# Performance work log

Measured on AMD Instinct MI355X. Metric: run time of the kernel, lower is better.

Reference implementation:

```python
import jax, jax.numpy as jnp
import numpy as np

B, S, D, H = 8, 1024, 1024, 16
DK = D // H
EPS = 1e-5

def _layernorm(x, w, b):
    mu = jnp.mean(x, axis=-1, keepdims=True)
    var = jnp.mean((x - mu) ** 2, axis=-1, keepdims=True)
    return (x - mu) * jax.lax.rsqrt(var + EPS) * w + b

def setup_inputs() -> dict:
    key = jax.random.key(0)
    ks = jax.random.split(key, 12)
    x = jax.random.normal(ks[0], (B, S, D), dtype=jnp.float32)
    batch_lengths = jax.random.randint(ks[1], (B,), S // 2, S + 1, dtype=jnp.int32)
    sc = 1.0 / np.sqrt(D)
    Wq = jax.random.normal(ks[2], (H, D, DK), dtype=jnp.float32) * sc
    Wk = jax.random.normal(ks[3], (H, D, DK), dtype=jnp.float32) * sc
    Wv = jax.random.normal(ks[4], (H, D, DK), dtype=jnp.float32) * sc
    fc1_w = jax.random.normal(ks[5], (D, D), dtype=jnp.float32) * sc
    fc1_b = jnp.zeros((D,), dtype=jnp.float32)
    fc2_w = jax.random.normal(ks[6], (D, D), dtype=jnp.float32) * sc
    fc2_b = jnp.zeros((D,), dtype=jnp.float32)
    ln1_w = jnp.ones((D,), dtype=jnp.float32)
    ln1_b = jnp.zeros((D,), dtype=jnp.float32)
    ln2_w = jnp.ones((D,), dtype=jnp.float32)
    ln2_b = jnp.zeros((D,), dtype=jnp.float32)
    return {"x": x, "Wq": Wq, "Wk": Wk, "Wv": Wv, "fc1_w": fc1_w, "fc1_b": fc1_b,
            "fc2_w": fc2_w, "fc2_b": fc2_b, "ln1_w": ln1_w, "ln1_b": ln1_b,
            "ln2_w": ln2_w, "ln2_b": ln2_b, "batch_lengths": batch_lengths, "max_len": S}

def reference(x, Wq, Wk, Wv, fc1_w, fc1_b, fc2_w, fc2_b, ln1_w, ln1_b, ln2_w, ln2_b, batch_lengths, max_len):
    b, s, d = x.shape
    h, _, dk = Wq.shape
    # padding masks: valid positions are t < length
    row = (jnp.arange(s)[None, :] < batch_lengths[:, None]).astype(x.dtype)  # [B,S]
    m = row[:, :, None]                 # [B,S,1], outputMask per-row
    mh = m[:, None]                     # [B,1,S,1]
    # all heads batched: Q,K,V -> [B,H,S,dk], masked like Wq(ctx)*mask etc.
    Q = jnp.einsum('bsd,hde->bhse', x, Wq) * mh
    K = jnp.einsum('bsd,hde->bhse', x, Wk) * mh
    V = jnp.einsum('bsd,hde->bhse', x, Wv) * mh
    energy = jnp.einsum('bhqe,bhke->bhqk', Q, K)
    # attnMask: key columns beyond length -> -inf
    key_valid = row[:, None, None, :] > 0
    energy = jnp.where(key_valid, energy, -jnp.inf)
    score = jax.nn.softmax(energy / jnp.sqrt(jnp.asarray(dk, x.dtype)), axis=-1)
    z = jnp.einsum('bhqk,bhke->bhqe', score, V)           # [B,H,S,dk]
    z = z.transpose(0, 2, 1, 3).reshape(b, s, d) * m      # concat heads, mask
    x1 = _layernorm(x + z, ln1_w, ln1_b)
    ff = jax.nn.relu(x1 @ fc1_w + fc1_b) * m
    ff = (ff @ fc2_w + fc2_b) * m
    return _layernorm(x1 + ff, ln2_w, ln2_b)
```

## Files before the change

### kernel.cpp

```cpp
#include <hip/hip_runtime.h>
#include <math.h>

#define B_ 8
#define S_ 1024
#define D_ 1024
#define H_ 16
#define DK_ 64
#define EPS_ 1e-5f

typedef __bf16 bf16_t;
typedef __bf16 bf16x8 __attribute__((ext_vector_type(8)));
typedef __bf16 bf16x4v __attribute__((ext_vector_type(4)));
typedef float  f32x4  __attribute__((ext_vector_type(4)));

__device__ __forceinline__ void gld16(const void* g, void* l) {
    __builtin_amdgcn_global_load_lds(
        (const __attribute__((address_space(1))) void*)g,
        (__attribute__((address_space(3))) void*)l, 16, 0, 0);
}

__global__ __launch_bounds__(256)
void prep(const float* __restrict__ x,
          const float* __restrict__ Wq, const float* __restrict__ Wk,
          const float* __restrict__ Wv, const float* __restrict__ W1,
          const float* __restrict__ W2, bf16_t* __restrict__ xb,
          bf16_t* __restrict__ WtQKV, bf16_t* __restrict__ Wt1,
          bf16_t* __restrict__ Wt2)
{
    __shared__ float tile[64][65];
    const int tid = threadIdx.x;
    const int z = blockIdx.z;

    if (z >= 5) {
        const int blk = (z - 5) * 256 + blockIdx.y * 16 + blockIdx.x;
        const int i = (blk * 256 + tid) * 4;
        const float4 v = *(const float4*)(x + i);
        bf16x4v o = { (bf16_t)v.x, (bf16_t)v.y, (bf16_t)v.z, (bf16_t)v.w };
        *(bf16x4v*)(xb + i) = o;
        return;
    }

    const int n0 = blockIdx.x * 64, k0 = blockIdx.y * 64;
    const int col = tid & 63, r0 = tid >> 6;
    const float* src = (z == 0) ? Wq : (z == 1) ? Wk : (z == 2) ? Wv
                     : (z == 3) ? W1 : W2;
    #pragma unroll
    for (int i = 0; i < 16; i++) {
        const int row = r0 + i * 4;
        float v;
        if (z < 3)
            v = src[((size_t)(n0 >> 6) << 16) + (size_t)(k0 + row) * 64 + col];
        else
            v = src[(size_t)(k0 + row) * D_ + n0 + col];
        tile[row][col] = v;
    }
    __syncthreads();
    bf16_t* dst = (z < 3) ? (WtQKV + (size_t)z * D_ * D_)
                : (z == 3) ? Wt1 : Wt2;
    #pragma unroll
    for (int i = 0; i < 16; i++) {
        const int nr = r0 + i * 4;
        dst[(size_t)(n0 + nr) * D_ + k0 + col] = (bf16_t)tile[col][nr];
    }
}

template<int EPI, typename OUT>
__global__ __launch_bounds__(256)
void gemm_mfma(const bf16_t* __restrict__ A, const bf16_t* __restrict__ Bw,
               const float* __restrict__ bias, const int* __restrict__ lens,
               OUT* __restrict__ C, int M, int N, int K)
{
    __shared__ bf16_t As[128 * 32];
    __shared__ bf16_t Bs[128 * 32];
    const int tid  = threadIdx.x;
    const int lane = tid & 63;
    const int w    = tid >> 6;
    const int quad = lane >> 4, l16 = lane & 15;
    const int wm = w & 1, wn = w >> 1;
    const int bn = blockIdx.x * 128, bm = blockIdx.y * 128;

    f32x4 acc[4][4];
    #pragma unroll
    for (int i = 0; i < 4; i++)
        #pragma unroll
        for (int j = 0; j < 4; j++)
            #pragma unroll
            for (int r = 0; r < 4; r++) acc[i][j][r] = 0.f;

    const int fsw = (quad ^ (l16 ^ (l16 >> 2))) & 3;

    for (int k0 = 0; k0 < K; k0 += 32) {
        #pragma unroll
        for (int j = 0; j < 2; j++) {
            const int chunk = j * 256 + tid;
            const int m = chunk >> 2, cs = chunk & 3;
            const int cg = cs ^ ((m ^ (m >> 2)) & 3);
            gld16(A + (size_t)(bm + m) * K + k0 + cg * 8,
                  (char*)As + (size_t)(j * 256 + w * 64) * 16);
            gld16(Bw + (size_t)(bn + m) * K + k0 + cg * 8,
                  (char*)Bs + (size_t)(j * 256 + w * 64) * 16);
        }
        __syncthreads();

        bf16x8 a[4], b[4];
        #pragma unroll
        for (int i = 0; i < 4; i++)
            a[i] = *(const bf16x8*)&As[(wm * 64 + i * 16 + l16) * 32 + fsw * 8];
        #pragma unroll
        for (int j = 0; j < 4; j++)
            b[j] = *(const bf16x8*)&Bs[(wn * 64 + j * 16 + l16) * 32 + fsw * 8];
        #pragma unroll
        for (int i = 0; i < 4; i++)
            #pragma unroll
            for (int j = 0; j < 4; j++)
                acc[i][j] = __builtin_amdgcn_mfma_f32_16x16x32_bf16(a[i], b[j], acc[i][j], 0, 0, 0);
        __syncthreads();
    }

    #pragma unroll
    for (int i = 0; i < 4; i++) {
        #pragma unroll
        for (int r = 0; r < 4; r++) {
            const int m = bm + wm * 64 + i * 16 + quad * 4 + r;
            float keep = 1.f;
            if (EPI != 0) {
                const int s = m & (S_ - 1);
                const int bb = m >> 10;
                keep = (s < lens[bb]) ? 1.f : 0.f;
            }
            #pragma unroll
            for (int j = 0; j < 4; j++) {
                const int n = bn + wn * 64 + j * 16 + l16;
                float v = acc[i][j][r];
                if (EPI != 0) {
                    v += bias[n];
                    if (EPI == 1) v = fmaxf(v, 0.f);
                    v *= keep;
                }
                C[(size_t)m * N + n] = (OUT)v;
            }
        }
    }
}

__global__ __launch_bounds__(256, 3)
void attn_mfma(const bf16_t* __restrict__ QKV, const int* __restrict__ lens,
               bf16_t* __restrict__ Z)
{
    __shared__ __align__(16) bf16_t Ks[2][64][64];
    __shared__ __align__(16) bf16_t Vt[2][64][72];
    __shared__ __align__(16) bf16_t Ps[64][72];

    const int tid  = threadIdx.x;
    const int lane = tid & 63;
    const int w    = tid >> 6;
    const int quad = lane >> 4;
    const int l16  = lane & 15;
    const int id   = blockIdx.x;
    const int b    = id & 7;
    const int h    = (id >> 3) & 15;
    const int qt   = id >> 7;
    const int len  = lens[b];
    const int qbase = qt * 64;
    const bf16_t* Qp = QKV + (size_t)b * S_ * 3072 + (size_t)h * 64;
    const bf16_t* Kp = Qp + 1024;
    const bf16_t* Vp = Qp + 2048;
    const size_t zbase = (size_t)b * S_ * D_ + (size_t)h * 64;

    if (qbase >= len) {
        const int r = tid >> 2, c0 = (tid & 3) * 16;
        bf16_t* zp = Z + zbase + (size_t)(qbase + r) * D_ + c0;
        uint4 zz = {0u, 0u, 0u, 0u};
        *(uint4*)zp = zz;
        *(uint4*)(zp + 8) = zz;
        return;
    }

    const int qrow = qbase + w * 16 + l16;
    const bf16x8 bq0 = *(const bf16x8*)(Qp + (size_t)qrow * 3072 + quad * 8);
    const bf16x8 bq1 = *(const bf16x8*)(Qp + (size_t)qrow * 3072 + 32 + quad * 8);

    const int kr0  = tid >> 3;
    const int kpos = tid & 7;
    const int kc0  = (kpos ^ (kr0 & 7)) << 3;
    const int kc1  = (kpos ^ ((kr0 + 32) & 7)) << 3;

    const int vr  = tid >> 2;
    const int vc0 = (tid & 3) * 16;
    const int vp  = vr ^ ((tid & 3) << 4);

    f32x4 o[4];
    #pragma unroll
    for (int dm = 0; dm < 4; dm++)
        #pragma unroll
        for (int r = 0; r < 4; r++) o[dm][r] = 0.f;
    float l_q = 0.f;

    const int ntiles = (len + 63) >> 6;

    gld16(Kp + (size_t)kr0 * 3072 + kc0,
          (char*)&Ks[0][0][0] + (size_t)(w * 64) * 16);
    gld16(Kp + (size_t)(kr0 + 32) * 3072 + kc1,
          (char*)&Ks[0][0][0] + (size_t)(256 + w * 64) * 16);
    bf16x8 vcur0 = *(const bf16x8*)(Vp + (size_t)vr * 3072 + vc0);
    bf16x8 vcur1 = *(const bf16x8*)(Vp + (size_t)vr * 3072 + vc0 + 8);
    __syncthreads();

    for (int t = 0; t < ntiles; t++) {
        const int k0 = t * 64;
        const int cb = t & 1, nb = (t + 1) & 1;
        const int kn0 = (t + 1 < ntiles ? t + 1 : t) * 64;

        gld16(Kp + (size_t)(kn0 + kr0) * 3072 + kc0,
              (char*)&Ks[nb][0][0] + (size_t)(w * 64) * 16);
        gld16(Kp + (size_t)(kn0 + kr0 + 32) * 3072 + kc1,
              (char*)&Ks[nb][0][0] + (size_t)(256 + w * 64) * 16);
        const bf16_t* vsrc = Vp + (size_t)(kn0 + vr) * 3072 + vc0;
        const bf16x8 vn0 = *(const bf16x8*)vsrc;
        const bf16x8 vn1 = *(const bf16x8*)(vsrc + 8);
        __builtin_amdgcn_sched_barrier(0);

        #pragma unroll
        for (int kt = 0; kt < 4; kt++) {
            const int r = kt * 16 + l16;
            const bf16x8 ak0 = *(const bf16x8*)&Ks[cb][r][(quad ^ (l16 & 7)) << 3];
            const bf16x8 ak1 = *(const bf16x8*)&Ks[cb][r][((4 + quad) ^ (l16 & 7)) << 3];
            f32x4 z4 = {0.f, 0.f, 0.f, 0.f};
            z4 = __builtin_amdgcn_mfma_f32_16x16x32_bf16(ak0, bq0, z4, 0, 0, 0);
            const f32x4 sfv = __builtin_amdgcn_mfma_f32_16x16x32_bf16(ak1, bq1, z4, 0, 0, 0);
            bf16x4v pk;
            #pragma unroll
            for (int r2 = 0; r2 < 4; r2++) {
                const int key = k0 + kt * 16 + quad * 4 + r2;
                float p = __expf(sfv[r2] * 0.125f);
                p = (key < len) ? p : 0.f;
                l_q += p;
                pk[r2] = (bf16_t)p;
            }
            *(bf16x4v*)&Ps[w * 16 + l16][kt * 16 + quad * 4] = pk;
        }

        #pragma unroll
        for (int i = 0; i < 8; i++) Vt[cb][vc0 + i][vp] = vcur0[i];
        #pragma unroll
        for (int i = 0; i < 8; i++) Vt[cb][vc0 + 8 + i][vp] = vcur1[i];
        vcur0 = vn0;
        vcur1 = vn1;
        __syncthreads();

        const bf16x8 bp0 = *(const bf16x8*)&Ps[w * 16 + l16][quad * 8];
        const bf16x8 bp1 = *(const bf16x8*)&Ps[w * 16 + l16][32 + quad * 8];
        #pragma unroll
        for (int dm = 0; dm < 4; dm++) {
            const bf16x8 av0 = *(const bf16x8*)&Vt[cb][dm * 16 + l16][(quad * 8) ^ (dm * 16)];
            const bf16x8 av1 = *(const bf16x8*)&Vt[cb][dm * 16 + l16][(32 + quad * 8) ^ (dm * 16)];
            o[dm] = __builtin_amdgcn_mfma_f32_16x16x32_bf16(av0, bp0, o[dm], 0, 0, 0);
            o[dm] = __builtin_amdgcn_mfma_f32_16x16x32_bf16(av1, bp1, o[dm], 0, 0, 0);
        }
    }

    l_q += __shfl_xor(l_q, 16);
    l_q += __shfl_xor(l_q, 32);
    const int qg = qbase + w * 16 + l16;
    const float inv = (qg < len) ? 1.f / l_q : 0.f;
    bf16_t* zrow = Z + zbase + (size_t)qg * D_;
    #pragma unroll
    for (int dm = 0; dm < 4; dm++) {
        bf16x4v st;
        #pragma unroll
        for (int r = 0; r < 4; r++) st[r] = (bf16_t)(o[dm][r] * inv);
        *(bf16x4v*)(zrow + dm * 16 + quad * 4) = st;
    }
}

__device__ __forceinline__ void ln_core(float vx, float vy, float vz, float vw,
                                        int tid, float& mean, float& rstd)
{
    __shared__ float red[8];
    float s = vx + vy + vz + vw;
    #pragma unroll
    for (int off = 32; off; off >>= 1) s += __shfl_xor(s, off, 64);
    const int wv = tid >> 6, lane = tid & 63;
    if (lane == 0) red[wv] = s;
    __syncthreads();
    mean = (red[0] + red[1] + red[2] + red[3]) * (1.f / D_);
    const float dx = vx - mean, dy = vy - mean, dz = vz - mean, dw = vw - mean;
    float s2 = dx * dx + dy * dy + dz * dz + dw * dw;
    #pragma unroll
    for (int off = 32; off; off >>= 1) s2 += __shfl_xor(s2, off, 64);
    if (lane == 0) red[4 + wv] = s2;
    __syncthreads();
    rstd = rsqrtf((red[4] + red[5] + red[6] + red[7]) * (1.f / D_) + EPS_);
}

__global__ __launch_bounds__(256)
void add_ln1(const float* __restrict__ X, const bf16_t* __restrict__ Y,
             const float* __restrict__ g, const float* __restrict__ beta,
             bf16_t* __restrict__ out)
{
    const int row = blockIdx.x, tid = threadIdx.x;
    const float4 xv = ((const float4*)(X + (size_t)row * D_))[tid];
    const bf16x4v yv = *(const bf16x4v*)(Y + (size_t)row * D_ + tid * 4);
    const float vx = xv.x + (float)yv[0], vy = xv.y + (float)yv[1];
    const float vz = xv.z + (float)yv[2], vw = xv.w + (float)yv[3];
    float mean, rstd;
    ln_core(vx, vy, vz, vw, tid, mean, rstd);
    const float4 gv = ((const float4*)g)[tid];
    const float4 bv = ((const float4*)beta)[tid];
    bf16x4v o;
    o[0] = (bf16_t)((vx - mean) * rstd * gv.x + bv.x);
    o[1] = (bf16_t)((vy - mean) * rstd * gv.y + bv.y);
    o[2] = (bf16_t)((vz - mean) * rstd * gv.z + bv.z);
    o[3] = (bf16_t)((vw - mean) * rstd * gv.w + bv.w);
    *(bf16x4v*)(out + (size_t)row * D_ + tid * 4) = o;
}

__global__ __launch_bounds__(256)
void add_ln2(const bf16_t* __restrict__ X, const float* __restrict__ Y,
             const float* __restrict__ g, const float* __restrict__ beta,
             float* __restrict__ out)
{
    const int row = blockIdx.x, tid = threadIdx.x;
    const bf16x4v xv = *(const bf16x4v*)(X + (size_t)row * D_ + tid * 4);
    const float4 yv = ((const float4*)(Y + (size_t)row * D_))[tid];
    const float vx = (float)xv[0] + yv.x, vy = (float)xv[1] + yv.y;
    const float vz = (float)xv[2] + yv.z, vw = (float)xv[3] + yv.w;
    float mean, rstd;
    ln_core(vx, vy, vz, vw, tid, mean, rstd);
    const float4 gv = ((const float4*)g)[tid];
    const float4 bv = ((const float4*)beta)[tid];
    float4 o;
    o.x = (vx - mean) * rstd * gv.x + bv.x;
    o.y = (vy - mean) * rstd * gv.y + bv.y;
    o.z = (vz - mean) * rstd * gv.z + bv.z;
    o.w = (vw - mean) * rstd * gv.w + bv.w;
    ((float4*)(out + (size_t)row * D_))[tid] = o;
}

extern "C" void kernel_launch(void* const* d_in, const int* in_sizes, int n_in,
                              void* d_out, int out_size, void* d_ws, size_t ws_size,
                              hipStream_t stream)
{
    const float* x    = (const float*)d_in[0];
    const float* Wq   = (const float*)d_in[1];
    const float* Wk   = (const float*)d_in[2];
    const float* Wv   = (const float*)d_in[3];
    const float* fc1w = (const float*)d_in[4];
    const float* fc1b = (const float*)d_in[5];
    const float* fc2w = (const float*)d_in[6];
    const float* fc2b = (const float*)d_in[7];
    const float* ln1w = (const float*)d_in[8];
    const float* ln1b = (const float*)d_in[9];
    const float* ln2w = (const float*)d_in[10];
    const float* ln2b = (const float*)d_in[11];
    const int*   lens = (const int*)d_in[12];
    float* out = (float*)d_out;

    char* ws = (char*)d_ws;
    const size_t MB = 1024 * 1024;
    bf16_t* QKVb  = (bf16_t*)(ws);
    bf16_t* Zb    = (bf16_t*)(ws + 48 * MB);
    bf16_t* X1b   = (bf16_t*)(ws + 80 * MB);
    bf16_t* xb    = (bf16_t*)(ws + 96 * MB);
    bf16_t* H1b   = (bf16_t*)(ws + 96 * MB);
    float*  FF    = (float*)(ws + 48 * MB);
    bf16_t* WtQKV = (bf16_t*)(ws + 112 * MB);
    bf16_t* Wt1   = (bf16_t*)(ws + 118 * MB);
    bf16_t* Wt2   = (bf16_t*)(ws + 120 * MB);

    const int M = B_ * S_;

    prep<<<dim3(16, 16, 37), 256, 0, stream>>>(x, Wq, Wk, Wv, fc1w, fc2w,
                                               xb, WtQKV, Wt1, Wt2);

    gemm_mfma<0, bf16_t><<<dim3(3072 / 128, M / 128), 256, 0, stream>>>(
        xb, WtQKV, nullptr, nullptr, QKVb, M, 3072, D_);

    attn_mfma<<<dim3(2048), 256, 0, stream>>>(QKVb, lens, Zb);

    add_ln1<<<M, 256, 0, stream>>>(x, Zb, ln1w, ln1b, X1b);

    gemm_mfma<1, bf16_t><<<dim3(D_ / 128, M / 128), 256, 0, stream>>>(
        X1b, Wt1, fc1b, lens, H1b, M, D_, D_);
    gemm_mfma<2, float><<<dim3(D_ / 128, M / 128), 256, 0, stream>>>(
        H1b, Wt2, fc2b, lens, FF, M, D_, D_);

    add_ln2<<<M, 256, 0, stream>>>(X1b, FF, ln2w, ln2b, out);
}
```

Before: 336.9 us.

## Replace GEMM with 256x256 double-buffered 8-wave pipelined MFMA kernel

Replaces the 128x128 single-buffered GEMM with a 256x256-tile, 512-thread kernel using BK=64. LDS is double-buffered with async global-to-LDS loads interleaved across four quarter-tile MFMA phases, with barrier and priority tricks. It aims to raise MFMA utilisation and hide load latency. In exchange it uses large LDS (limiting occupancy) and launches far fewer blocks, which underfills the CUs for the D×D FFN GEMMs.

```diff
diff --git a/kernel.cpp b/kernel.cpp
--- a/kernel.cpp
+++ b/kernel.cpp
@@ -65,63 +65,139 @@
 }
 
 template<int EPI, typename OUT>
-__global__ __launch_bounds__(256)
-void gemm_mfma(const bf16_t* __restrict__ A, const bf16_t* __restrict__ Bw,
-               const float* __restrict__ bias, const int* __restrict__ lens,
-               OUT* __restrict__ C, int M, int N, int K)
-{
-    __shared__ bf16_t As[128 * 32];
-    __shared__ bf16_t Bs[128 * 32];
+__global__ __launch_bounds__(512, 2)
+void gemm8(const bf16_t* __restrict__ A, const bf16_t* __restrict__ Bw,
+           const float* __restrict__ bias, const int* __restrict__ lens,
+           OUT* __restrict__ C, int M, int N, int K)
+{
+    __shared__ __align__(16) bf16_t As[2][256 * 64];
+    __shared__ __align__(16) bf16_t Bs[2][256 * 64];
+
     const int tid  = threadIdx.x;
     const int lane = tid & 63;
     const int w    = tid >> 6;
     const int quad = lane >> 4, l16 = lane & 15;
     const int wm = w & 1, wn = w >> 1;
-    const int bn = blockIdx.x * 128, bm = blockIdx.y * 128;
-
-    f32x4 acc[4][4];
-    #pragma unroll
-    for (int i = 0; i < 4; i++)
+    const int bn = blockIdx.x * 256, bm = blockIdx.y * 256;
+    const int sw8 = l16 & 7;
+
+    const int ci0 = tid, ci1 = tid + 512;
+    const int aB0 = ci0 >> 9, aR0 = (ci0 >> 3) & 63;
+    const int aC0 = (((ci0 & 7) ^ (aR0 & 7)) << 3);
+    const int aB1 = ci1 >> 9, aR1 = (ci1 >> 3) & 63;
+    const int aC1 = (((ci1 & 7) ^ (aR1 & 7)) << 3);
+    const int bB0 = ci0 >> 8, bR0 = (ci0 >> 3) & 31;
+    const int bC0 = (((ci0 & 7) ^ (bR0 & 7)) << 3);
+    const int bB1 = ci1 >> 8, bR1 = (ci1 >> 3) & 31;
+    const int bC1 = (((ci1 & 7) ^ (bR1 & 7)) << 3);
+    const int u0 = w * 64, u1 = 512 + w * 64;
+    const int adD0 = (u0 >> 9) * 16384 + (u0 & 511) * 16;
+    const int adD1 = (u1 >> 9) * 16384 + (u1 & 511) * 16;
+    const int bdD0 = (u0 >> 8) * 8192 + (u0 & 255) * 16;
+    const int bdD1 = (u1 >> 8) * 8192 + (u1 & 255) * 16;
+
+    f32x4 acc[8][4];
+    #pragma unroll
+    for (int i = 0; i < 8; i++)
         #pragma unroll
         for (int j = 0; j < 4; j++)
             #pragma unroll
             for (int r = 0; r < 4; r++) acc[i][j][r] = 0.f;
 
-    const int fsw = (quad ^ (l16 ^ (l16 >> 2))) & 3;
-
-    for (int k0 = 0; k0 < K; k0 += 32) {
-        #pragma unroll
-        for (int j = 0; j < 2; j++) {
-            const int chunk = j * 256 + tid;
-            const int m = chunk >> 2, cs = chunk & 3;
-            const int cg = cs ^ ((m ^ (m >> 2)) & 3);
-            gld16(A + (size_t)(bm + m) * K + k0 + cg * 8,
-                  (char*)As + (size_t)(j * 256 + w * 64) * 16);
-            gld16(Bw + (size_t)(bn + m) * K + k0 + cg * 8,
-                  (char*)Bs + (size_t)(j * 256 + w * 64) * 16);
-        }
-        __syncthreads();
-
-        bf16x8 a[4], b[4];
-        #pragma unroll
-        for (int i = 0; i < 4; i++)
-            a[i] = *(const bf16x8*)&As[(wm * 64 + i * 16 + l16) * 32 + fsw * 8];
-        #pragma unroll
-        for (int j = 0; j < 4; j++)
-            b[j] = *(const bf16x8*)&Bs[(wn * 64 + j * 16 + l16) * 32 + fsw * 8];
-        #pragma unroll
-        for (int i = 0; i < 4; i++)
-            #pragma unroll
-            for (int j = 0; j < 4; j++)
-                acc[i][j] = __builtin_amdgcn_mfma_f32_16x16x32_bf16(a[i], b[j], acc[i][j], 0, 0, 0);
-        __syncthreads();
-    }
-
-    #pragma unroll
-    for (int i = 0; i < 4; i++) {
+#define STAGE_A(h, nb_, kt_) { \
+    char* d_ = (char*)As[nb_] + (h) * 8192; \
+    gld16(A + (size_t)(bm + aB0 * 128 + (h) * 64 + aR0) * K + (kt_) * 64 + aC0, d_ + adD0); \
+    gld16(A + (size_t)(bm + aB1 * 128 + (h) * 64 + aR1) * K + (kt_) * 64 + aC1, d_ + adD1); }
+#define STAGE_B(h, nb_, kt_) { \
+    char* d_ = (char*)Bs[nb_] + (h) * 4096; \
+    gld16(Bw + (size_t)(bn + bB0 * 64 + (h) * 32 + bR0) * K + (kt_) * 64 + bC0, d_ + bdD0); \
+    gld16(Bw + (size_t)(bn + bB1 * 64 + (h) * 32 + bR1) * K + (kt_) * 64 + bC1, d_ + bdD1); }
+#define RD_A(dst, base, qm_, i_, kh_) \
+    dst = *(const bf16x8*)&base[(wm * 128 + (qm_) * 64 + (i_) * 16 + l16) * 64 + ((((kh_) * 4 + quad) ^ sw8) << 3)];
+#define RD_B(dst, base, qn_, j_, kh_) \
+    dst = *(const bf16x8*)&base[(wn * 64 + (qn_) * 32 + (j_) * 16 + l16) * 64 + ((((kh_) * 4 + quad) ^ sw8) << 3)];
+#define MM(QI, QJ, AF, BF) \
+    _Pragma("unroll") \
+    for (int kh_ = 0; kh_ < 2; kh_++) \
+        _Pragma("unroll") \
+        for (int i_ = 0; i_ < 4; i_++) \
+            _Pragma("unroll") \
+            for (int j_ = 0; j_ < 2; j_++) \
+                acc[(QI) * 4 + i_][(QJ) * 2 + j_] = __builtin_amdgcn_mfma_f32_16x16x32_bf16( \
+                    AF[i_][kh_], BF[j_][kh_], acc[(QI) * 4 + i_][(QJ) * 2 + j_], 0, 0, 0);
+#define MIDBAR() { __builtin_amdgcn_s_barrier(); \
+    asm volatile("s_waitcnt lgkmcnt(0)" ::: "memory"); }
+
+    const int NKT = K >> 6;
+
+    STAGE_A(0, 0, 0);
+    STAGE_B(0, 0, 0);
+    STAGE_B(1, 0, 0);
+    STAGE_A(1, 0, 0);
+    asm volatile("s_waitcnt vmcnt(4)" ::: "memory");
+    __builtin_amdgcn_s_barrier();
+
+    for (int t = 0; t < NKT; ++t) {
+        const int cb = t & 1, nb = cb ^ 1;
+        const int ktn = (t + 1 < NKT) ? t + 1 : t;
+        const bf16_t* Ac = As[cb];
+        const bf16_t* Bc = Bs[cb];
+
+        bf16x8 fa[4][2], fb[2][2];
+        #pragma unroll
+        for (int i = 0; i < 4; i++) { RD_A(fa[i][0], Ac, 0, i, 0); RD_A(fa[i][1], Ac, 0, i, 1); }
+        #pragma unroll
+        for (int j = 0; j < 2; j++) { RD_B(fb[j][0], Bc, 0, j, 0); RD_B(fb[j][1], Bc, 0, j, 1); }
+        STAGE_A(0, nb, ktn);
+        MIDBAR();
+        __builtin_amdgcn_s_setprio(1);
+        MM(0, 0, fa, fb);
+        __builtin_amdgcn_s_setprio(0);
+        asm volatile("s_waitcnt vmcnt(4)" ::: "memory");
+        __builtin_amdgcn_s_barrier();
+
+        bf16x8 gb[2][2];
+        #pragma unroll
+        for (int j = 0; j < 2; j++) { RD_B(gb[j][0], Bc, 1, j, 0); RD_B(gb[j][1], Bc, 1, j, 1); }
+        STAGE_B(0, nb, ktn);
+        MIDBAR();
+        __builtin_amdgcn_s_setprio(1);
+        MM(0, 1, fa, gb);
+        __builtin_amdgcn_s_setprio(0);
+        asm volatile("s_waitcnt vmcnt(4)" ::: "memory");
+        __builtin_amdgcn_s_barrier();
+
+        bf16x8 ga[4][2];
+        #pragma unroll
+        for (int i = 0; i < 4; i++) { RD_A(ga[i][0], Ac, 1, i, 0); RD_A(ga[i][1], Ac, 1, i, 1); }
+        STAGE_B(1, nb, ktn);
+        MIDBAR();
+        __builtin_amdgcn_s_setprio(1);
+        MM(1, 1, ga, gb);
+        __builtin_amdgcn_s_setprio(0);
+        __builtin_amdgcn_s_barrier();
+
+        STAGE_A(1, nb, ktn);
+        MIDBAR();
+        __builtin_amdgcn_s_setprio(1);
+        MM(1, 0, ga, fb);
+        __builtin_amdgcn_s_setprio(0);
+        asm volatile("s_waitcnt vmcnt(4)" ::: "memory");
+        __builtin_amdgcn_s_barrier();
+    }
+
+#undef STAGE_A
+#undef STAGE_B
+#undef RD_A
+#undef RD_B
+#undef MM
+#undef MIDBAR
+
+    #pragma unroll
+    for (int ii = 0; ii < 8; ii++) {
         #pragma unroll
         for (int r = 0; r < 4; r++) {
-            const int m = bm + wm * 64 + i * 16 + quad * 4 + r;
+            const int m = bm + wm * 128 + (ii >> 2) * 64 + (ii & 3) * 16 + quad * 4 + r;
             float keep = 1.f;
             if (EPI != 0) {
                 const int s = m & (S_ - 1);
@@ -129,9 +205,9 @@
                 keep = (s < lens[bb]) ? 1.f : 0.f;
             }
             #pragma unroll
-            for (int j = 0; j < 4; j++) {
-                const int n = bn + wn * 64 + j * 16 + l16;
-                float v = acc[i][j][r];
+            for (int jj = 0; jj < 4; jj++) {
+                const int n = bn + wn * 64 + (jj >> 1) * 32 + (jj & 1) * 16 + l16;
+                float v = acc[ii][jj][r];
                 if (EPI != 0) {
                     v += bias[n];
                     if (EPI == 1) v = fmaxf(v, 0.f);
@@ -373,16 +449,16 @@
     prep<<<dim3(16, 16, 37), 256, 0, stream>>>(x, Wq, Wk, Wv, fc1w, fc2w,
                                                xb, WtQKV, Wt1, Wt2);
 
-    gemm_mfma<0, bf16_t><<<dim3(3072 / 128, M / 128), 256, 0, stream>>>(
+    gemm8<0, bf16_t><<<dim3(3072 / 256, M / 256), 512, 0, stream>>>(
         xb, WtQKV, nullptr, nullptr, QKVb, M, 3072, D_);
 
     attn_mfma<<<dim3(2048), 256, 0, stream>>>(QKVb, lens, Zb);
 
     add_ln1<<<M, 256, 0, stream>>>(x, Zb, ln1w, ln1b, X1b);
 
-    gemm_mfma<1, bf16_t><<<dim3(D_ / 128, M / 128), 256, 0, stream>>>(
+    gemm8<1, bf16_t><<<dim3(D_ / 256, M / 256), 512, 0, stream>>>(
         X1b, Wt1, fc1b, lens, H1b, M, D_, D_);
-    gemm_mfma<2, float><<<dim3(D_ / 128, M / 128), 256, 0, stream>>>(
+    gemm8<2, float><<<dim3(D_ / 256, M / 256), 512, 0, stream>>>(
         H1b, Wt2, fc2b, lens, FF, M, D_, D_);
 
     add_ln2<<<M, 256, 0, stream>>>(X1b, FF, ln2w, ln2b, out);
```

New measurement: 347.7 us. +3.2%, slower.

## Pre-pack GEMM weights into MFMA fragments and double-buffer A tiles in LDS

Applied to the files above, without the earlier changes.

The prep kernel now writes the weight matrices in a packed 16x8 fragment layout, so each lane can load its B operand straight from global memory into registers and skip LDS. The GEMM uses a 64-wide K step with double-buffered A tiles in LDS, prefetching the next tile while the current one feeds the MFMAs, and synchronises with one barrier per step plus a partial vmcnt wait. It also remaps workgroup IDs for better L2 locality and requests two blocks per CU. In exchange, register pressure rises from holding two sets of B fragments, and B global loads are no longer shared across waves through LDS.

```diff
diff --git a/kernel.cpp b/kernel.cpp
--- a/kernel.cpp
+++ b/kernel.cpp
@@ -60,24 +60,41 @@
     #pragma unroll
     for (int i = 0; i < 16; i++) {
         const int nr = r0 + i * 4;
-        dst[(size_t)(n0 + nr) * D_ + k0 + col] = (bf16_t)tile[col][nr];
+        const int n = n0 + nr, k = k0 + col;
+        const size_t pidx = ((size_t)(n >> 4) * (D_ >> 3) + (k >> 3)) * 128
+                          + (size_t)(n & 15) * 8 + (k & 7);
+        dst[pidx] = (bf16_t)tile[col][nr];
     }
 }
 
 template<int EPI, typename OUT>
-__global__ __launch_bounds__(256)
-void gemm_mfma(const bf16_t* __restrict__ A, const bf16_t* __restrict__ Bw,
-               const float* __restrict__ bias, const int* __restrict__ lens,
-               OUT* __restrict__ C, int M, int N, int K)
-{
-    __shared__ bf16_t As[128 * 32];
-    __shared__ bf16_t Bs[128 * 32];
+__global__ __launch_bounds__(256, 2)
+void gemm_bp(const bf16_t* __restrict__ A, const bf16_t* __restrict__ Bp,
+             const float* __restrict__ bias, const int* __restrict__ lens,
+             OUT* __restrict__ C, int M, int N, int K)
+{
+    __shared__ __align__(16) bf16_t As[2][128 * 64];
+
     const int tid  = threadIdx.x;
     const int lane = tid & 63;
     const int w    = tid >> 6;
     const int quad = lane >> 4, l16 = lane & 15;
     const int wm = w & 1, wn = w >> 1;
-    const int bn = blockIdx.x * 128, bm = blockIdx.y * 128;
+    const int sw8 = l16 & 7;
+
+    const int nwg  = gridDim.x * gridDim.y;
+    const int orig = blockIdx.y * gridDim.x + blockIdx.x;
+    const int swz  = (orig & 7) * (nwg >> 3) + (orig >> 3);
+    const int bn = (swz % gridDim.x) * 128;
+    const int bm = (swz / gridDim.x) * 128;
+
+    const int rS  = tid >> 3;
+    const int cS  = ((tid & 7) ^ (rS & 7)) << 3;
+    const int dOf = w * 1024;
+
+    const size_t ntStride = (size_t)(K >> 3) * 128;
+    const bf16_t* Bw = Bp + ((size_t)(bn >> 4) + (size_t)wn * 4) * ntStride
+                          + (size_t)quad * 128 + (size_t)l16 * 8;
 
     f32x4 acc[4][4];
     #pragma unroll
@@ -87,35 +104,58 @@
             #pragma unroll
             for (int r = 0; r < 4; r++) acc[i][j][r] = 0.f;
 
-    const int fsw = (quad ^ (l16 ^ (l16 >> 2))) & 3;
-
-    for (int k0 = 0; k0 < K; k0 += 32) {
-        #pragma unroll
-        for (int j = 0; j < 2; j++) {
-            const int chunk = j * 256 + tid;
-            const int m = chunk >> 2, cs = chunk & 3;
-            const int cg = cs ^ ((m ^ (m >> 2)) & 3);
-            gld16(A + (size_t)(bm + m) * K + k0 + cg * 8,
-                  (char*)As + (size_t)(j * 256 + w * 64) * 16);
-            gld16(Bw + (size_t)(bn + m) * K + k0 + cg * 8,
-                  (char*)Bs + (size_t)(j * 256 + w * 64) * 16);
-        }
-        __syncthreads();
-
-        bf16x8 a[4], b[4];
-        #pragma unroll
-        for (int i = 0; i < 4; i++)
-            a[i] = *(const bf16x8*)&As[(wm * 64 + i * 16 + l16) * 32 + fsw * 8];
-        #pragma unroll
-        for (int j = 0; j < 4; j++)
-            b[j] = *(const bf16x8*)&Bs[(wn * 64 + j * 16 + l16) * 32 + fsw * 8];
-        #pragma unroll
-        for (int i = 0; i < 4; i++)
-            #pragma unroll
-            for (int j = 0; j < 4; j++)
-                acc[i][j] = __builtin_amdgcn_mfma_f32_16x16x32_bf16(a[i], b[j], acc[i][j], 0, 0, 0);
-        __syncthreads();
-    }
+#define SA(b_, kt_) { \
+    _Pragma("unroll") \
+    for (int s_ = 0; s_ < 4; s_++) \
+        gld16(A + (size_t)(bm + s_ * 32 + rS) * K + (kt_) * 64 + cS, \
+              (char*)As[b_] + s_ * 4096 + dOf); }
+#define LB(dst_, kt_) { \
+    _Pragma("unroll") \
+    for (int j_ = 0; j_ < 4; j_++) \
+        _Pragma("unroll") \
+        for (int kh_ = 0; kh_ < 2; kh_++) \
+            dst_[j_][kh_] = *(const bf16x8*)(Bw + (size_t)j_ * ntStride \
+                                             + ((kt_) * 8 + kh_ * 4) * 128); }
+#define KSTEP(cb_, nb_, BC_, BX_, t_) { \
+    const int ktn_ = ((t_) + 1 < NKT) ? (t_) + 1 : (t_); \
+    SA(nb_, ktn_); \
+    LB(BX_, ktn_); \
+    __builtin_amdgcn_sched_barrier(0); \
+    const bf16_t* Ac = As[cb_]; \
+    _Pragma("unroll") \
+    for (int kh_ = 0; kh_ < 2; kh_++) { \
+        bf16x8 a_[4]; \
+        _Pragma("unroll") \
+        for (int i_ = 0; i_ < 4; i_++) \
+            a_[i_] = *(const bf16x8*)&Ac[(wm * 64 + i_ * 16 + l16) * 64 \
+                                         + (((kh_ * 4 + quad) ^ sw8) << 3)]; \
+        _Pragma("unroll") \
+        for (int i_ = 0; i_ < 4; i_++) \
+            _Pragma("unroll") \
+            for (int j_ = 0; j_ < 4; j_++) \
+                acc[i_][j_] = __builtin_amdgcn_mfma_f32_16x16x32_bf16( \
+                    a_[i_], BC_[j_][kh_], acc[i_][j_], 0, 0, 0); \
+    } \
+    __builtin_amdgcn_sched_barrier(0); \
+    asm volatile("s_waitcnt vmcnt(8)" ::: "memory"); \
+    __builtin_amdgcn_s_barrier(); }
+
+    const int NKT = K >> 6;
+
+    bf16x8 bA[4][2], bB[4][2];
+    SA(0, 0);
+    LB(bA, 0);
+    asm volatile("s_waitcnt vmcnt(8)" ::: "memory");
+    __builtin_amdgcn_s_barrier();
+
+    for (int t = 0; t < NKT; t += 2) {
+        KSTEP(0, 1, bA, bB, t);
+        KSTEP(1, 0, bB, bA, t + 1);
+    }
+
+#undef SA
+#undef LB
+#undef KSTEP
 
     #pragma unroll
     for (int i = 0; i < 4; i++) {
@@ -373,16 +413,16 @@
     prep<<<dim3(16, 16, 37), 256, 0, stream>>>(x, Wq, Wk, Wv, fc1w, fc2w,
                                                xb, WtQKV, Wt1, Wt2);
 
-    gemm_mfma<0, bf16_t><<<dim3(3072 / 128, M / 128), 256, 0, stream>>>(
+    gemm_bp<0, bf16_t><<<dim3(3072 / 128, M / 128), 256, 0, stream>>>(
         xb, WtQKV, nullptr, nullptr, QKVb, M, 3072, D_);
 
     attn_mfma<<<dim3(2048), 256, 0, stream>>>(QKVb, lens, Zb);
 
     add_ln1<<<M, 256, 0, stream>>>(x, Zb, ln1w, ln1b, X1b);
 
-    gemm_mfma<1, bf16_t><<<dim3(D_ / 128, M / 128), 256, 0, stream>>>(
+    gemm_bp<1, bf16_t><<<dim3(D_ / 128, M / 128), 256, 0, stream>>>(
         X1b, Wt1, fc1b, lens, H1b, M, D_, D_);
-    gemm_mfma<2, float><<<dim3(D_ / 128, M / 128), 256, 0, stream>>>(
+    gemm_bp<2, float><<<dim3(D_ / 128, M / 128), 256, 0, stream>>>(
         H1b, Wt2, fc2b, lens, FF, M, D_, D_);
 
     add_ln2<<<M, 256, 0, stream>>>(X1b, FF, ln2w, ln2b, out);
```

After: 310.6 us. 7.8% less time.
